# Kernel tuning notes

Measured on AMD Instinct MI355X. Metric: run time of the kernel, lower is better.

The kernel has to match this reference:

```python
import jax, jax.numpy as jnp
import numpy as np

N_IN, N_OUT, N_TO = 64, 64, 16  # connection table: each output plane gets N_TO random input planes
K = N_OUT * N_TO                # 1024 connections
KH, KW = 3, 3
B, H, W = 4, 192, 192


def setup_inputs() -> dict:
    key = jax.random.key(0)
    kx, kw_, kb, kc = jax.random.split(key, 4)
    x = jax.random.normal(kx, (B, N_IN, H, W), dtype=jnp.float32)
    weight = jax.random.normal(kw_, (K, KH, KW), dtype=jnp.float32) * (1.0 / np.sqrt(KH * KW * N_TO))
    bias = jax.random.normal(kb, (N_OUT,), dtype=jnp.float32) * 0.01
    # maps.random semantics: each output plane j has exactly N_TO input connections
    conn_in = jax.random.randint(kc, (K,), 0, N_IN, dtype=jnp.int32)
    conn_out = jnp.repeat(jnp.arange(N_OUT, dtype=jnp.int32), N_TO)
    return {"x": x, "weight": weight, "bias": bias, "conn_in": conn_in, "conn_out": conn_out}


def reference(x, weight, bias, conn_in, conn_out):
    # x: [B, nIn, H, W]; weight: [K, kH, kW]; connection k convolves plane conn_in[k]
    # into plane conn_out[k] with its own kernel (valid conv, stride 1).
    nK = weight.shape[0]
    nOut = bias.shape[0]
    xg = x[:, conn_in]                       # [B, K, H, W] gather input planes per connection
    y = jax.lax.conv_general_dilated(
        xg, weight[:, None],                 # kernel [K, 1, kH, kW], grouped => per-connection conv
        window_strides=(1, 1), padding='VALID',
        feature_group_count=nK,
        dimension_numbers=('NCHW', 'OIHW', 'NCHW'))  # [B, K, Ho, Wo]
    # scatter-add connections into their output planes
    out = jax.ops.segment_sum(jnp.moveaxis(y, 1, 0), conn_out, num_segments=nOut)  # [nOut, B, Ho, Wo]
    return jnp.moveaxis(out, 0, 1) + bias[None, :, None, None]
```

## Files before the change

kernel.cpp:

```cpp
#include <hip/hip_runtime.h>
#include <hip/hip_bf16.h>

#define HH 192
#define WW 192
#define HOUT 190
#define NCH 64
#define W2_N (64 * 9 * 64)

typedef __attribute__((ext_vector_type(8))) short bf16x8;
typedef __attribute__((ext_vector_type(4))) float f32x4;

static __device__ __forceinline__ ushort f2bf(float f) {
    __hip_bfloat16 h = __float2bfloat16(f);
    return *reinterpret_cast<ushort*>(&h);
}
static __device__ __forceinline__ uint pack2bf(float lo, float hi) {
    return (uint)f2bf(lo) | ((uint)f2bf(hi) << 16);
}

__global__ __launch_bounds__(256) void build_w2(const float* __restrict__ w,
                                                const int* __restrict__ conn,
                                                ushort* __restrict__ w2) {
    int idx = blockIdx.x * 256 + threadIdx.x;
    if (idx >= W2_N) return;
    int o = idx / 576, rem = idx - o * 576, tap = rem >> 6, c = rem & 63;
    float s = 0.f;
    #pragma unroll
    for (int t = 0; t < 16; ++t) {
        int k = o * 16 + t;
        if (conn[k] == c) s += w[k * 9 + tap];
    }
    w2[idx] = f2bf(s);
}

__global__ __launch_bounds__(256, 3) void scm_mfma(
    const float* __restrict__ x,
    const ushort* __restrict__ w2,
    const float* __restrict__ bias,
    float* __restrict__ out)
{
    __shared__ ushort xt[10 * 18 * 72];

    const int tid  = threadIdx.x;
    const int lane = tid & 63;
    const int wv   = tid >> 6;
    const int col  = lane & 15;
    const int g    = lane >> 4;

    const int bid = blockIdx.x;
    const int lid = (bid & 7) * 144 + (bid >> 3);
    const int b      = lid / 288;
    const int tileid = lid % 288;
    const int ti0 = (tileid / 12) * 8;
    const int tj0 = (tileid % 12) * 16;

    {
        const int srr  = lane / 18;
        const int scol = lane - srr * 18;
        const bool act = lane < 54;
        int gc = tj0 + scol; if (gc > 191) gc = 191;
        int gr0 = ti0 + srr;     if (gr0 > 191) gr0 = 191;
        int gr1 = ti0 + srr + 3; if (gr1 > 191) gr1 = 191;
        int gr2 = ti0 + srr + 6; if (gr2 > 191) gr2 = 191;
        int gr3 = ti0 + srr + 9; if (gr3 > 191) gr3 = 191;

        #pragma unroll
        for (int pass = 0; pass < 2; ++pass) {
            float v[8][4];
            #pragma unroll
            for (int pj = 0; pj < 8; ++pj) {
                const int c = wv * 16 + pass * 8 + pj;
                const float* xc = x + ((size_t)(b * NCH + c)) * (HH * WW);
                v[pj][0] = xc[gr0 * WW + gc];
                v[pj][1] = xc[gr1 * WW + gc];
                v[pj][2] = xc[gr2 * WW + gc];
                v[pj][3] = xc[gr3 * WW + gc];
            }
            __builtin_amdgcn_sched_barrier(0);
            if (act) {
                #pragma unroll
                for (int pp = 0; pp < 4; ++pp) {
                    const int c = wv * 16 + pass * 8 + 2 * pp;
                    uint k0 = pack2bf(v[2 * pp][0], v[2 * pp + 1][0]);
                    uint k1 = pack2bf(v[2 * pp][1], v[2 * pp + 1][1]);
                    uint k2 = pack2bf(v[2 * pp][2], v[2 * pp + 1][2]);
                    uint k3 = pack2bf(v[2 * pp][3], v[2 * pp + 1][3]);
                    *(uint*)&xt[((srr    ) * 18 + scol) * 72 + c] = k0;
                    *(uint*)&xt[((srr + 3) * 18 + scol) * 72 + c] = k1;
                    *(uint*)&xt[((srr + 6) * 18 + scol) * 72 + c] = k2;
                    if (srr == 0)
                        *(uint*)&xt[(9 * 18 + scol) * 72 + c] = k3;
                }
            }
        }
    }
    __syncthreads();

    f32x4 acc[8];
    #pragma unroll
    for (int i = 0; i < 8; ++i) acc[i] = (f32x4){0.f, 0.f, 0.f, 0.f};

    const ushort* ap0 = &xt[col * 72 + g * 8];
    const ushort* bp  = w2 + (16 * wv + col) * 576 + g * 8;

    bf16x8 fA[10], fB[10];
    bf16x8 Bs[9];

#define LOADB(s) do {                                                          \
        _Pragma("unroll")                                                      \
        for (int _tap = 0; _tap < 9; ++_tap)                                   \
            Bs[_tap] = *(const bf16x8*)(bp + _tap * 64 + (s) * 32);            \
    } while (0)

#define LOADF(F, s, kw) do {                                                   \
        _Pragma("unroll")                                                      \
        for (int _R = 0; _R < 10; ++_R)                                        \
            F[_R] = *(const bf16x8*)(ap0 + (_R * 18 + (kw)) * 72 + (s) * 32);  \
    } while (0)

#define MFMA24(F, kw) do {                                                     \
        _Pragma("unroll")                                                      \
        for (int _Mt = 0; _Mt < 8; ++_Mt) {                                    \
            acc[_Mt] = __builtin_amdgcn_mfma_f32_16x16x32_bf16(Bs[kw],     F[_Mt],     acc[_Mt], 0, 0, 0); \
            acc[_Mt] = __builtin_amdgcn_mfma_f32_16x16x32_bf16(Bs[3+(kw)], F[_Mt + 1], acc[_Mt], 0, 0, 0); \
            acc[_Mt] = __builtin_amdgcn_mfma_f32_16x16x32_bf16(Bs[6+(kw)], F[_Mt + 2], acc[_Mt], 0, 0, 0); \
        }                                                                      \
    } while (0)

    LOADB(0);
    LOADF(fA, 0, 0);
    LOADF(fB, 0, 1);  MFMA24(fA, 0);
    LOADF(fA, 0, 2);  MFMA24(fB, 1);
    LOADF(fB, 1, 0);  MFMA24(fA, 2);
    LOADB(1);
    LOADF(fA, 1, 1);  MFMA24(fB, 0);
    LOADF(fB, 1, 2);  MFMA24(fA, 1);
    MFMA24(fB, 2);

#undef LOADB
#undef LOADF
#undef MFMA24

    const int pcol = tj0 + col;
    const int obase = 16 * wv + 4 * g;
    float bv[4];
    #pragma unroll
    for (int reg = 0; reg < 4; ++reg) bv[reg] = bias[obase + reg];

    if (pcol < HOUT) {
        #pragma unroll
        for (int Mt = 0; Mt < 8; ++Mt) {
            const int row = ti0 + Mt;
            if (row < HOUT) {
                float* rp = out + ((size_t)(b * NCH + obase) * HOUT + row) * HOUT + pcol;
                #pragma unroll
                for (int reg = 0; reg < 4; ++reg)
                    rp[(size_t)reg * HOUT * HOUT] = acc[Mt][reg] + bv[reg];
            }
        }
    }
}

extern "C" void kernel_launch(void* const* d_in, const int* in_sizes, int n_in,
                              void* d_out, int out_size, void* d_ws, size_t ws_size,
                              hipStream_t stream) {
    const float* x       = (const float*)d_in[0];
    const float* weight  = (const float*)d_in[1];
    const float* bias    = (const float*)d_in[2];
    const int*   conn_in = (const int*)d_in[3];

    ushort* w2 = (ushort*)d_ws;

    build_w2<<<dim3((W2_N + 255) / 256), dim3(256), 0, stream>>>(weight, conn_in, w2);

    scm_mfma<<<dim3(1152), dim3(256), 0, stream>>>(x, w2, bias, (float*)d_out);
}
```

Measured before the change: 33.78 us.

## Halve output tile height to 4 rows and double block count

Shrinks each block's output tile from 8x16 to 4x16 pixels, which halves shared memory (6 halo rows instead of 10), halves the accumulator and fragment registers, and doubles the grid to 2304 blocks. Weight fragments are now loaded per kernel column in double-buffered triples, interleaved with the MFMA groups, instead of all nine taps at once. This is meant to raise occupancy and parallelism. In exchange the halo overhead grows (6 loaded rows for 4 output rows versus 10 for 8), so global reads of x and weight reloads per output increase.

```diff
diff --git a/kernel.cpp b/kernel.cpp
--- a/kernel.cpp
+++ b/kernel.cpp
@@ -39,7 +39,7 @@
     const float* __restrict__ bias,
     float* __restrict__ out)
 {
-    __shared__ ushort xt[10 * 18 * 72];
+    __shared__ ushort xt[6 * 18 * 72];
 
     const int tid  = threadIdx.x;
     const int lane = tid & 63;
@@ -48,10 +48,10 @@
     const int g    = lane >> 4;
 
     const int bid = blockIdx.x;
-    const int lid = (bid & 7) * 144 + (bid >> 3);
-    const int b      = lid / 288;
-    const int tileid = lid % 288;
-    const int ti0 = (tileid / 12) * 8;
+    const int lid = (bid & 7) * 288 + (bid >> 3);
+    const int b      = lid / 576;
+    const int tileid = lid % 576;
+    const int ti0 = (tileid / 12) * 4;
     const int tj0 = (tileid % 12) * 16;
 
     {
@@ -61,85 +61,71 @@
         int gc = tj0 + scol; if (gc > 191) gc = 191;
         int gr0 = ti0 + srr;     if (gr0 > 191) gr0 = 191;
         int gr1 = ti0 + srr + 3; if (gr1 > 191) gr1 = 191;
-        int gr2 = ti0 + srr + 6; if (gr2 > 191) gr2 = 191;
-        int gr3 = ti0 + srr + 9; if (gr3 > 191) gr3 = 191;
 
+        float v[16][2];
         #pragma unroll
-        for (int pass = 0; pass < 2; ++pass) {
-            float v[8][4];
+        for (int j = 0; j < 16; ++j) {
+            const int c = wv * 16 + j;
+            const float* xc = x + ((size_t)(b * NCH + c)) * (HH * WW);
+            v[j][0] = xc[gr0 * WW + gc];
+            v[j][1] = xc[gr1 * WW + gc];
+        }
+        __builtin_amdgcn_sched_barrier(0);
+        if (act) {
             #pragma unroll
-            for (int pj = 0; pj < 8; ++pj) {
-                const int c = wv * 16 + pass * 8 + pj;
-                const float* xc = x + ((size_t)(b * NCH + c)) * (HH * WW);
-                v[pj][0] = xc[gr0 * WW + gc];
-                v[pj][1] = xc[gr1 * WW + gc];
-                v[pj][2] = xc[gr2 * WW + gc];
-                v[pj][3] = xc[gr3 * WW + gc];
-            }
-            __builtin_amdgcn_sched_barrier(0);
-            if (act) {
-                #pragma unroll
-                for (int pp = 0; pp < 4; ++pp) {
-                    const int c = wv * 16 + pass * 8 + 2 * pp;
-                    uint k0 = pack2bf(v[2 * pp][0], v[2 * pp + 1][0]);
-                    uint k1 = pack2bf(v[2 * pp][1], v[2 * pp + 1][1]);
-                    uint k2 = pack2bf(v[2 * pp][2], v[2 * pp + 1][2]);
-                    uint k3 = pack2bf(v[2 * pp][3], v[2 * pp + 1][3]);
-                    *(uint*)&xt[((srr    ) * 18 + scol) * 72 + c] = k0;
-                    *(uint*)&xt[((srr + 3) * 18 + scol) * 72 + c] = k1;
-                    *(uint*)&xt[((srr + 6) * 18 + scol) * 72 + c] = k2;
-                    if (srr == 0)
-                        *(uint*)&xt[(9 * 18 + scol) * 72 + c] = k3;
-                }
+            for (int pp = 0; pp < 8; ++pp) {
+                const int c = wv * 16 + 2 * pp;
+                uint k0 = pack2bf(v[2 * pp][0], v[2 * pp + 1][0]);
+                uint k1 = pack2bf(v[2 * pp][1], v[2 * pp + 1][1]);
+                *(uint*)&xt[((srr    ) * 18 + scol) * 72 + c] = k0;
+                *(uint*)&xt[((srr + 3) * 18 + scol) * 72 + c] = k1;
             }
         }
     }
     __syncthreads();
 
-    f32x4 acc[8];
+    f32x4 acc[4];
     #pragma unroll
-    for (int i = 0; i < 8; ++i) acc[i] = (f32x4){0.f, 0.f, 0.f, 0.f};
+    for (int i = 0; i < 4; ++i) acc[i] = (f32x4){0.f, 0.f, 0.f, 0.f};
 
     const ushort* ap0 = &xt[col * 72 + g * 8];
     const ushort* bp  = w2 + (16 * wv + col) * 576 + g * 8;
 
-    bf16x8 fA[10], fB[10];
-    bf16x8 Bs[9];
+    bf16x8 fA[6], fB[6];
+    bf16x8 BA[3], BB[3];
 
-#define LOADB(s) do {                                                          \
+#define LOADB(B, s, kw) do {                                                   \
         _Pragma("unroll")                                                      \
-        for (int _tap = 0; _tap < 9; ++_tap)                                   \
-            Bs[_tap] = *(const bf16x8*)(bp + _tap * 64 + (s) * 32);            \
+        for (int _j = 0; _j < 3; ++_j)                                         \
+            B[_j] = *(const bf16x8*)(bp + (_j * 3 + (kw)) * 64 + (s) * 32);    \
     } while (0)
 
 #define LOADF(F, s, kw) do {                                                   \
         _Pragma("unroll")                                                      \
-        for (int _R = 0; _R < 10; ++_R)                                        \
+        for (int _R = 0; _R < 6; ++_R)                                         \
             F[_R] = *(const bf16x8*)(ap0 + (_R * 18 + (kw)) * 72 + (s) * 32);  \
     } while (0)
 
-#define MFMA24(F, kw) do {                                                     \
+#define MFMA12(F, B) do {                                                      \
         _Pragma("unroll")                                                      \
-        for (int _Mt = 0; _Mt < 8; ++_Mt) {                                    \
-            acc[_Mt] = __builtin_amdgcn_mfma_f32_16x16x32_bf16(Bs[kw],     F[_Mt],     acc[_Mt], 0, 0, 0); \
-            acc[_Mt] = __builtin_amdgcn_mfma_f32_16x16x32_bf16(Bs[3+(kw)], F[_Mt + 1], acc[_Mt], 0, 0, 0); \
-            acc[_Mt] = __builtin_amdgcn_mfma_f32_16x16x32_bf16(Bs[6+(kw)], F[_Mt + 2], acc[_Mt], 0, 0, 0); \
+        for (int _Mt = 0; _Mt < 4; ++_Mt) {                                    \
+            acc[_Mt] = __builtin_amdgcn_mfma_f32_16x16x32_bf16(B[0], F[_Mt],     acc[_Mt], 0, 0, 0); \
+            acc[_Mt] = __builtin_amdgcn_mfma_f32_16x16x32_bf16(B[1], F[_Mt + 1], acc[_Mt], 0, 0, 0); \
+            acc[_Mt] = __builtin_amdgcn_mfma_f32_16x16x32_bf16(B[2], F[_Mt + 2], acc[_Mt], 0, 0, 0); \
         }                                                                      \
     } while (0)
 
-    LOADB(0);
-    LOADF(fA, 0, 0);
-    LOADF(fB, 0, 1);  MFMA24(fA, 0);
-    LOADF(fA, 0, 2);  MFMA24(fB, 1);
-    LOADF(fB, 1, 0);  MFMA24(fA, 2);
-    LOADB(1);
-    LOADF(fA, 1, 1);  MFMA24(fB, 0);
-    LOADF(fB, 1, 2);  MFMA24(fA, 1);
-    MFMA24(fB, 2);
+    LOADB(BA, 0, 0);  LOADF(fA, 0, 0);
+    LOADB(BB, 0, 1);  LOADF(fB, 0, 1);  MFMA12(fA, BA);
+    LOADB(BA, 0, 2);  LOADF(fA, 0, 2);  MFMA12(fB, BB);
+    LOADB(BB, 1, 0);  LOADF(fB, 1, 0);  MFMA12(fA, BA);
+    LOADB(BA, 1, 1);  LOADF(fA, 1, 1);  MFMA12(fB, BB);
+    LOADB(BB, 1, 2);  LOADF(fB, 1, 2);  MFMA12(fA, BA);
+    MFMA12(fB, BB);
 
 #undef LOADB
 #undef LOADF
-#undef MFMA24
+#undef MFMA12
 
     const int pcol = tj0 + col;
     const int obase = 16 * wv + 4 * g;
@@ -149,7 +135,7 @@
 
     if (pcol < HOUT) {
         #pragma unroll
-        for (int Mt = 0; Mt < 8; ++Mt) {
+        for (int Mt = 0; Mt < 4; ++Mt) {
             const int row = ti0 + Mt;
             if (row < HOUT) {
                 float* rp = out + ((size_t)(b * NCH + obase) * HOUT + row) * HOUT + pcol;
@@ -173,5 +159,5 @@
 
     build_w2<<<dim3((W2_N + 255) / 256), dim3(256), 0, stream>>>(weight, conn_in, w2);
 
-    scm_mfma<<<dim3(1152), dim3(256), 0, stream>>>(x, w2, bias, (float*)d_out);
+    scm_mfma<<<dim3(2304), dim3(256), 0, stream>>>(x, w2, bias, (float*)d_out);
 }
```

Result: slower. 40.78 us (+20.7%).
